# Kernel optimization log

Measured on AMD Instinct MI355X. Metric: run time of the kernel, lower is better.

Reference implementation:

```python
import jax, jax.numpy as jnp
import numpy as np

IN_DIM, OUT_DIM, NUM, K = 256, 256, 8, 3
BATCH = 2048
GRID_LO, GRID_HI = -1.0, 1.0


def _basis_matrix(k):
    # Uniform B-spline basis matrix, exact translation of MatrixKANLayer.basis_matrix
    M = np.array([[1.0]], dtype=np.float64)
    scalar = 1.0
    for kk in range(2, k + 2):
        t1 = np.vstack([M, np.zeros((1, M.shape[1]))])
        t3 = np.vstack([np.zeros((1, M.shape[1])), M])
        t2 = np.zeros((kk - 1, kk))
        t4 = np.zeros((kk - 1, kk))
        for i in range(kk - 1):
            t2[i, i] = i + 1
            t2[i, i + 1] = kk - (i + 2)
            t4[i, i] = -1.0
            t4[i, i + 1] = 1.0
        M = t1 @ t2 + t3 @ t4
        scalar *= 1.0 / (kk - 1)
    return (M * scalar).astype(np.float32)

BASIS = jnp.asarray(_basis_matrix(K))  # (K+1, K+1); rows indexed by power of u


def setup_inputs() -> dict:
    key = jax.random.key(0)
    kx, kc, kb = jax.random.split(key, 3)
    x = jax.random.normal(kx, (BATCH, IN_DIM), dtype=jnp.float32)
    # learned params sized per __init__: coef (in, out, num+k), scales/mask (in, out)
    coef = jax.random.normal(kc, (IN_DIM, OUT_DIM, NUM + K), dtype=jnp.float32) * (0.5 / NUM)
    scale_base = ((jax.random.uniform(kb, (IN_DIM, OUT_DIM), dtype=jnp.float32) * 2.0 - 1.0)
                  / np.sqrt(IN_DIM).astype(np.float32))
    scale_sp = jnp.ones((IN_DIM, OUT_DIM), dtype=jnp.float32)
    mask = jnp.ones((IN_DIM, OUT_DIM), dtype=jnp.float32)
    return {"x": x, "coef": coef, "scale_base": scale_base, "scale_sp": scale_sp, "mask": mask}


def reference(x, coef, scale_base, scale_sp, mask):
    shift = (GRID_LO + GRID_HI) / 2.0           # layer_norm_shifts (per-dim, all equal)
    scal = (GRID_HI - GRID_LO) / 2.0            # layer_norm_scalars
    # tanh squash into grid range: x = tanh((x-shift)/(scal/2))*scal + shift
    xn = jnp.tanh((x - shift) / (scal / 2.0)) * scal + shift
    B = xn.shape[0]
    preacts = jnp.broadcast_to(xn[:, None, :], (B, OUT_DIM, IN_DIM))
    base = xn * jax.nn.sigmoid(xn)              # SiLU residual function

    # --- matrix-form B-spline evaluation ---
    h = (GRID_HI - GRID_LO) / NUM               # uniform grid interval
    pos = (xn - GRID_LO) / h
    fidx = jnp.clip(jnp.floor(pos), 0.0, NUM - 1)
    u = pos - fidx                              # normalized offset in [0,1)
    idx = fidx.astype(jnp.int32)                # interval index -> coef window start
    # power bases [1, u, u^2, ..., u^K]; avoid u**0 for clean grads
    powers = jnp.stack([jnp.ones_like(u)] + [u ** j for j in range(1, K + 1)], axis=-1)
    vals = powers @ BASIS                       # (B, I, K+1) basis function values
    # scatter basis values into full (num+k)-length basis vector per (b, i)
    win = idx[..., None] + jnp.arange(K + 1)    # (B, I, K+1) coef indices
    onehot = jax.nn.one_hot(win, NUM + K, dtype=vals.dtype)  # (B, I, K+1, NUM+K)
    full = jnp.einsum('bij,bijn->bin', vals, onehot)         # (B, I, NUM+K)
    spl = jnp.einsum('bin,ion->bio', full, coef)             # (B, I, O)

    postspline = jnp.transpose(spl, (0, 2, 1))
    y = scale_base[None, :, :] * base[:, :, None] + scale_sp[None, :, :] * spl
    y = mask[None, :, :] * y
    postacts = jnp.transpose(y, (0, 2, 1))
    y = jnp.sum(y, axis=1)                      # (B, O)
    return y, preacts, postacts, postspline
```

## Files before the change

kernel.cpp:

```cpp
#include <hip/hip_runtime.h>

#define BATCH 2048
#define IN    256
#define OUTD  256
#define NC    11
#define SC    32
#define TW    33

typedef __attribute__((ext_vector_type(4))) float f32x4;
typedef __attribute__((ext_vector_type(2))) float f32x2;

#define LDS_BARRIER()                                              \
    do {                                                           \
        asm volatile("s_waitcnt lgkmcnt(0)" ::: "memory");         \
        __builtin_amdgcn_s_barrier();                              \
    } while (0)

__global__ __launch_bounds__(256) void build_tables(
    const float* __restrict__ coef, const float* __restrict__ sb,
    const float* __restrict__ ss, const float* __restrict__ mk,
    f32x4* __restrict__ coefQ, f32x2* __restrict__ msbmss)
{
    const int i = blockIdx.x;
    const int o = threadIdx.x;
    const float* src = coef + ((size_t)i * OUTD + o) * NC;
    float c[NC];
    #pragma unroll
    for (int n = 0; n < NC; ++n) c[n] = src[n];
    #pragma unroll
    for (int n0 = 0; n0 < 8; ++n0) {
        f32x4 q;
        q.x = c[n0]; q.y = c[n0 + 1]; q.z = c[n0 + 2]; q.w = c[n0 + 3];
        coefQ[((size_t)i * 8 + n0) * OUTD + o] = q;
    }
    const int io = i * OUTD + o;
    const float m = mk[io];
    f32x2 ms; ms.x = m * sb[io]; ms.y = m * ss[io];
    msbmss[io] = ms;
}

__global__ __launch_bounds__(256, 3) void kan_main(
    const float* __restrict__ x, const f32x4* __restrict__ coefQ,
    const f32x2* __restrict__ msbmss, float* __restrict__ out)
{
    __shared__ f32x4 v_s[IN];
    __shared__ float base_s[IN];
    __shared__ int   comb_s[IN];
    __shared__ float xn_s[IN];
    __shared__ float tile[OUTD * TW];

    const int b = blockIdx.x;
    const int t = threadIdx.x;

    {
        float xv  = x[(size_t)b * IN + t];
        float xn  = tanhf(2.0f * xv);
        float sig = 1.0f / (1.0f + expf(-xn));
        float base = xn * sig;
        float pos  = (xn + 1.0f) * 4.0f;
        float fidx = fminf(fmaxf(floorf(pos), 0.0f), 7.0f);
        float u    = pos - fidx;
        int   idx  = (int)fidx;
        float u2 = u * u, u3 = u2 * u;
        const float c6 = 1.0f / 6.0f;
        f32x4 v;
        v.x = (1.0f - 3.0f * u + 3.0f * u2 - u3) * c6;
        v.y = (4.0f - 6.0f * u2 + 3.0f * u3) * c6;
        v.z = (1.0f + 3.0f * u + 3.0f * u2 - 3.0f * u3) * c6;
        v.w = u3 * c6;
        v_s[t]    = v;
        base_s[t] = base;
        comb_s[t] = (t * 8 + idx) * OUTD;
        xn_s[t]   = xn;
    }
    __syncthreads();

    float* y    = out;
    float* pre  = out + (size_t)BATCH * OUTD;
    float* pact = pre  + (size_t)BATCH * OUTD * IN;
    float* pspl = pact + (size_t)BATCH * OUTD * IN;

    {
        f32x4 myxn = ((const f32x4*)xn_s)[t & 63];
        f32x4* dst = (f32x4*)(pre + (size_t)b * OUTD * IN);
        #pragma unroll 8
        for (int c = 0; c < 64; ++c)
            __builtin_nontemporal_store(myxn, dst + c * 256 + t);
    }

    float yacc = 0.0f;
    const int o = t;
    const size_t bbase = (size_t)b * OUTD * IN;

    for (int s = 0; s < IN / SC; ++s) {
        const int i0 = s * SC;
        float yfr[SC];

        #pragma unroll
        for (int ii = 0; ii < SC; ++ii) {
            const int i = i0 + ii;
            f32x4 q = coefQ[comb_s[i] + o];
            f32x2 m = msbmss[i * OUTD + o];
            f32x4 v = v_s[i];
            float spl = q.x * v.x + q.y * v.y + q.z * v.z + q.w * v.w;
            float yf  = m.x * base_s[i] + m.y * spl;
            yacc += yf;
            tile[o * TW + ii] = spl;
            yfr[ii] = yf;
        }
        LDS_BARRIER();

        #pragma unroll
        for (int c = 0; c < 8; ++c) {
            const int f   = c * 256 + t;
            const int row = f >> 3;
            const int q8  = f & 7;
            const int la  = row * TW + q8 * 4;
            f32x4 vv;
            vv.x = tile[la]; vv.y = tile[la+1]; vv.z = tile[la+2]; vv.w = tile[la+3];
            const size_t g = bbase + (size_t)row * IN + i0 + q8 * 4;
            __builtin_nontemporal_store(vv, (f32x4*)(pspl + g));
        }
        LDS_BARRIER();

        #pragma unroll
        for (int ii = 0; ii < SC; ++ii) tile[o * TW + ii] = yfr[ii];
        LDS_BARRIER();

        #pragma unroll
        for (int c = 0; c < 8; ++c) {
            const int f   = c * 256 + t;
            const int row = f >> 3;
            const int q8  = f & 7;
            const int la  = row * TW + q8 * 4;
            f32x4 vv;
            vv.x = tile[la]; vv.y = tile[la+1]; vv.z = tile[la+2]; vv.w = tile[la+3];
            const size_t g = bbase + (size_t)row * IN + i0 + q8 * 4;
            __builtin_nontemporal_store(vv, (f32x4*)(pact + g));
        }
        LDS_BARRIER();
    }

    y[(size_t)b * OUTD + o] = yacc;
}

__global__ __launch_bounds__(256, 3) void kan_main_direct(
    const float* __restrict__ x, const float* __restrict__ coef,
    const float* __restrict__ sb, const float* __restrict__ ss,
    const float* __restrict__ mk, float* __restrict__ out)
{
    __shared__ f32x4 v_s[IN];
    __shared__ float base_s[IN];
    __shared__ int   comb_s[IN];
    __shared__ float xn_s[IN];
    __shared__ float ps_t[OUTD * 17];
    __shared__ float pa_t[OUTD * 17];

    const int b = blockIdx.x;
    const int t = threadIdx.x;
    {
        float xv  = x[(size_t)b * IN + t];
        float xn  = tanhf(2.0f * xv);
        float sig = 1.0f / (1.0f + expf(-xn));
        float base = xn * sig;
        float pos  = (xn + 1.0f) * 4.0f;
        float fidx = fminf(fmaxf(floorf(pos), 0.0f), 7.0f);
        float u    = pos - fidx;
        int   idx  = (int)fidx;
        float u2 = u * u, u3 = u2 * u;
        const float c6 = 1.0f / 6.0f;
        f32x4 v;
        v.x = (1.0f - 3.0f * u + 3.0f * u2 - u3) * c6;
        v.y = (4.0f - 6.0f * u2 + 3.0f * u3) * c6;
        v.z = (1.0f + 3.0f * u + 3.0f * u2 - 3.0f * u3) * c6;
        v.w = u3 * c6;
        v_s[t] = v; base_s[t] = base;
        comb_s[t] = t * (OUTD * NC) + idx;
        xn_s[t] = xn;
    }
    __syncthreads();

    float* y    = out;
    float* pre  = out + (size_t)BATCH * OUTD;
    float* pact = pre  + (size_t)BATCH * OUTD * IN;
    float* pspl = pact + (size_t)BATCH * OUTD * IN;
    {
        f32x4 myxn = ((const f32x4*)xn_s)[t & 63];
        f32x4* dst = (f32x4*)(pre + (size_t)b * OUTD * IN);
        #pragma unroll 8
        for (int c = 0; c < 64; ++c)
            __builtin_nontemporal_store(myxn, dst + c * 256 + t);
    }
    float yacc = 0.0f;
    const int o = t;
    const int oNC = o * NC;
    const size_t bbase = (size_t)b * OUTD * IN;
    for (int ic = 0; ic < 16; ++ic) {
        #pragma unroll
        for (int ii = 0; ii < 16; ++ii) {
            const int i = ic * 16 + ii;
            f32x4 v = v_s[i];
            const float* cp = coef + comb_s[i] + oNC;
            float spl = cp[0] * v.x + cp[1] * v.y + cp[2] * v.z + cp[3] * v.w;
            const int io = i * OUTD + o;
            float yf = mk[io] * (sb[io] * base_s[i] + ss[io] * spl);
            yacc += yf;
            ps_t[o * 17 + ii] = spl;
            pa_t[o * 17 + ii] = yf;
        }
        LDS_BARRIER();
        #pragma unroll
        for (int c = 0; c < 4; ++c) {
            const int f  = c * 256 + t;
            const int oo = f >> 2;
            const int i4 = (f & 3) * 4;
            const int la = oo * 17 + i4;
            f32x4 vps, vpa;
            vps.x = ps_t[la]; vps.y = ps_t[la+1]; vps.z = ps_t[la+2]; vps.w = ps_t[la+3];
            vpa.x = pa_t[la]; vpa.y = pa_t[la+1]; vpa.z = pa_t[la+2]; vpa.w = pa_t[la+3];
            const size_t g = bbase + (size_t)oo * IN + ic * 16 + i4;
            __builtin_nontemporal_store(vps, (f32x4*)(pspl + g));
            __builtin_nontemporal_store(vpa, (f32x4*)(pact + g));
        }
        LDS_BARRIER();
    }
    y[(size_t)b * OUTD + o] = yacc;
}

extern "C" void kernel_launch(void* const* d_in, const int* in_sizes, int n_in,
                              void* d_out, int out_size, void* d_ws, size_t ws_size,
                              hipStream_t stream) {
    const float* x    = (const float*)d_in[0];
    const float* coef = (const float*)d_in[1];
    const float* sb   = (const float*)d_in[2];
    const float* ss   = (const float*)d_in[3];
    const float* mk   = (const float*)d_in[4];
    float* out = (float*)d_out;

    const size_t coefQ_bytes  = (size_t)IN * 8 * OUTD * sizeof(f32x4);
    const size_t msbmss_bytes = (size_t)IN * OUTD * sizeof(f32x2);

    if (ws_size >= coefQ_bytes + msbmss_bytes) {
        f32x4* coefQ  = (f32x4*)d_ws;
        f32x2* msbmss = (f32x2*)((char*)d_ws + coefQ_bytes);
        build_tables<<<IN, 256, 0, stream>>>(coef, sb, ss, mk, coefQ, msbmss);
        kan_main<<<BATCH, 256, 0, stream>>>(x, coefQ, msbmss, out);
    } else {
        kan_main_direct<<<BATCH, 256, 0, stream>>>(x, coef, sb, ss, mk, out);
    }
}
```

Baseline: 349.0 us.

## Tile main KAN kernel by output chunks so stores write contiguous rows

Reorganizes kan_main to iterate over 8 chunks of 32 output features, with each thread covering 32 inputs for one output, instead of iterating over input slices. Each chunk writes full contiguous 1 KB rows of postspline, postacts and preacts rather than scattered 128-byte segments, which is meant to improve write coalescing and DRAM efficiency for the memory-bound output. Preacts stores are now interleaved with the postspline stores. The y sum becomes a cross-group LDS reduction, which adds a little extra LDS traffic. Coef gather locality also changes, since neighbouring threads now read different input rows.

```diff
diff --git a/kernel.cpp b/kernel.cpp
--- a/kernel.cpp
+++ b/kernel.cpp
@@ -4,8 +4,8 @@
 #define IN    256
 #define OUTD  256
 #define NC    11
-#define SC    32
-#define TW    33
+#define OC    32
+#define TS    257
 
 typedef __attribute__((ext_vector_type(4))) float f32x4;
 typedef __attribute__((ext_vector_type(2))) float f32x2;
@@ -47,7 +47,8 @@
     __shared__ float base_s[IN];
     __shared__ int   comb_s[IN];
     __shared__ float xn_s[IN];
-    __shared__ float tile[OUTD * TW];
+    __shared__ float yp_s[8][32];
+    __shared__ float tile[OC * TS];
 
     const int b = blockIdx.x;
     const int t = threadIdx.x;
@@ -80,68 +81,76 @@
     float* pact = pre  + (size_t)BATCH * OUTD * IN;
     float* pspl = pact + (size_t)BATCH * OUTD * IN;
 
-    {
-        f32x4 myxn = ((const f32x4*)xn_s)[t & 63];
-        f32x4* dst = (f32x4*)(pre + (size_t)b * OUTD * IN);
-        #pragma unroll 8
-        for (int c = 0; c < 64; ++c)
-            __builtin_nontemporal_store(myxn, dst + c * 256 + t);
-    }
-
-    float yacc = 0.0f;
-    const int o = t;
+    const int og = t & 31;
+    const int ig = t >> 5;
     const size_t bbase = (size_t)b * OUTD * IN;
 
-    for (int s = 0; s < IN / SC; ++s) {
-        const int i0 = s * SC;
-        float yfr[SC];
-
-        #pragma unroll
-        for (int ii = 0; ii < SC; ++ii) {
-            const int i = i0 + ii;
+    for (int oc = 0; oc < 8; ++oc) {
+        const int obase = oc * OC;
+        const int o = obase + og;
+        float yfr[32];
+        float yp = 0.0f;
+
+        #pragma unroll
+        for (int st = 0; st < 32; ++st) {
+            const int i = ig * 32 + st;
             f32x4 q = coefQ[comb_s[i] + o];
             f32x2 m = msbmss[i * OUTD + o];
             f32x4 v = v_s[i];
             float spl = q.x * v.x + q.y * v.y + q.z * v.z + q.w * v.w;
             float yf  = m.x * base_s[i] + m.y * spl;
-            yacc += yf;
-            tile[o * TW + ii] = spl;
-            yfr[ii] = yf;
-        }
-        LDS_BARRIER();
-
-        #pragma unroll
-        for (int c = 0; c < 8; ++c) {
-            const int f   = c * 256 + t;
-            const int row = f >> 3;
-            const int q8  = f & 7;
-            const int la  = row * TW + q8 * 4;
-            f32x4 vv;
-            vv.x = tile[la]; vv.y = tile[la+1]; vv.z = tile[la+2]; vv.w = tile[la+3];
-            const size_t g = bbase + (size_t)row * IN + i0 + q8 * 4;
-            __builtin_nontemporal_store(vv, (f32x4*)(pspl + g));
-        }
-        LDS_BARRIER();
-
-        #pragma unroll
-        for (int ii = 0; ii < SC; ++ii) tile[o * TW + ii] = yfr[ii];
-        LDS_BARRIER();
-
-        #pragma unroll
-        for (int c = 0; c < 8; ++c) {
-            const int f   = c * 256 + t;
-            const int row = f >> 3;
-            const int q8  = f & 7;
-            const int la  = row * TW + q8 * 4;
-            f32x4 vv;
-            vv.x = tile[la]; vv.y = tile[la+1]; vv.z = tile[la+2]; vv.w = tile[la+3];
-            const size_t g = bbase + (size_t)row * IN + i0 + q8 * 4;
-            __builtin_nontemporal_store(vv, (f32x4*)(pact + g));
-        }
-        LDS_BARRIER();
-    }
-
-    y[(size_t)b * OUTD + o] = yacc;
+            yp += yf;
+            tile[og * TS + i] = spl;
+            yfr[st] = yf;
+        }
+        yp_s[ig][og] = yp;
+        LDS_BARRIER();
+
+        {
+            f32x4* psplR = (f32x4*)(pspl + bbase + (size_t)obase * IN);
+            f32x4* preR  = (f32x4*)(pre  + bbase + (size_t)obase * IN);
+            #pragma unroll
+            for (int c = 0; c < 8; ++c) {
+                const int idx = c * 256 + t;
+                const int row = idx >> 6;
+                const int c4  = idx & 63;
+                const int la  = row * TS + c4 * 4;
+                f32x4 vv;
+                vv.x = tile[la];   vv.y = tile[la+1];
+                vv.z = tile[la+2]; vv.w = tile[la+3];
+                __builtin_nontemporal_store(vv, psplR + idx);
+                f32x4 xv = ((const f32x4*)xn_s)[c4];
+                __builtin_nontemporal_store(xv, preR + idx);
+            }
+            if (t < 32) {
+                float s = 0.0f;
+                #pragma unroll
+                for (int g = 0; g < 8; ++g) s += yp_s[g][t];
+                y[(size_t)b * OUTD + obase + t] = s;
+            }
+        }
+        LDS_BARRIER();
+
+        #pragma unroll
+        for (int st = 0; st < 32; ++st) tile[og * TS + ig * 32 + st] = yfr[st];
+        LDS_BARRIER();
+
+        {
+            f32x4* pactR = (f32x4*)(pact + bbase + (size_t)obase * IN);
+            #pragma unroll
+            for (int c = 0; c < 8; ++c) {
+                const int idx = c * 256 + t;
+                const int row = idx >> 6;
+                const int c4  = idx & 63;
+                const int la  = row * TS + c4 * 4;
+                f32x4 vv;
+                vv.x = tile[la];   vv.y = tile[la+1];
+                vv.z = tile[la+2]; vv.w = tile[la+3];
+                __builtin_nontemporal_store(vv, pactR + idx);
+            }
+        }
+        LDS_BARRIER();
+    }
 }
 
 __global__ __launch_bounds__(256, 3) void kan_main_direct(
```

New measurement: 333.9 us. -4.3%, faster.
